# Optimization experiments

Measured on AMD Instinct MI355X. Metric: run time of the kernel, lower is better.

The kernel has to match this reference:

```python
import jax, jax.numpy as jnp
import numpy as np

B, GS, IN_H, GCN_H, LIN_H = 65536, 7, 5, 144, 128


def _xavier(key, shape):
    fan_in, fan_out = shape[0], shape[1]
    limit = np.sqrt(6.0 / (fan_in + fan_out)).astype(np.float32)
    return jax.random.uniform(key, shape, jnp.float32, -limit, limit)


def setup_inputs() -> dict:
    key = jax.random.key(0)
    ks = jax.random.split(key, 12)
    operations = jax.random.normal(ks[0], (B, GS, IN_H), jnp.float32)
    adjacency = (jax.random.uniform(ks[1], (B, GS, GS)) < 0.3).astype(jnp.float32)
    num_vertices = jax.random.randint(ks[2], (B,), 1, 8).astype(jnp.float32)
    w1_0 = _xavier(ks[3], (IN_H, GCN_H))
    w2_0 = _xavier(ks[4], (IN_H, GCN_H))
    w1_1 = _xavier(ks[5], (GCN_H, GCN_H))
    w2_1 = _xavier(ks[6], (GCN_H, GCN_H))
    w1_2 = _xavier(ks[7], (GCN_H, GCN_H))
    w2_2 = _xavier(ks[8], (GCN_H, GCN_H))
    fc1_w = _xavier(ks[9], (LIN_H, GCN_H))  # torch Linear stores [out, in]
    fc2_w = _xavier(ks[10], (1, LIN_H))
    return {
        'operations': operations, 'adjacency': adjacency, 'num_vertices': num_vertices,
        'w1_0': w1_0, 'w2_0': w2_0, 'w1_1': w1_1, 'w2_1': w2_1,
        'w1_2': w1_2, 'w2_2': w2_2, 'fc1_w': fc1_w, 'fc2_w': fc2_w,
    }


def _row_normalize(adj):
    # divide each row by its sum (matches torch normalize_adj)
    return adj / adj.sum(axis=2, keepdims=True)


def reference(operations, adjacency, num_vertices,
              w1_0, w2_0, w1_1, w2_1, w1_2, w2_2, fc1_w, fc2_w):
    gs = adjacency.shape[1]
    eye = jnp.eye(gs, dtype=adjacency.dtype)
    adj_d = _row_normalize(adjacency + eye)  # [B, gs, gs]
    x = operations
    for w1, w2 in ((w1_0, w2_0), (w1_1, w2_1), (w1_2, w2_2)):
        norm_adj = _row_normalize(adj_d)                      # identity in value, kept faithful
        inv_norm_adj = _row_normalize(adj_d.transpose(0, 2, 1))
        o1 = jax.nn.relu(jnp.einsum('bij,bjk->bik', norm_adj, x @ w1))
        o2 = jax.nn.relu(jnp.einsum('bij,bjk->bik', inv_norm_adj, x @ w2))
        x = (o1 + o2) * 0.5  # dropout is identity at inference
    pooled = x.sum(axis=1) / num_vertices[:, None]            # [B, gcn_hidden]
    h = pooled @ fc1_w.T                                      # [B, linear_hidden]
    out = (h @ fc2_w.T).reshape(-1)                           # [B]
    return out
```

## Files before the change

### kernel.cpp

```cpp
#include <hip/hip_runtime.h>


typedef _Float16 half8   __attribute__((ext_vector_type(8)));
typedef _Float16 half4_t __attribute__((ext_vector_type(4)));
typedef float    floatx16 __attribute__((ext_vector_type(16)));

constexpr int GS = 7;
constexpr int NI = 8;
constexpr int MROWS = NI * GS;
constexpr int H = 144;
constexpr int LSTRIDE = 2 * 5 * 9 * 512;
constexpr int WT_HALFS = 3 * LSTRIDE;
constexpr int FRAGS = 3 * 90 * 64;

static __device__ inline half8 bc(_Float16 v) {
    half8 h = {v, v, v, v, v, v, v, v};
    return h;
}

__global__ void prep_kernel(const float* __restrict__ w10, const float* __restrict__ w20,
                            const float* __restrict__ w11, const float* __restrict__ w21,
                            const float* __restrict__ w12, const float* __restrict__ w22,
                            const float* __restrict__ fc1, const float* __restrict__ fc2,
                            _Float16* __restrict__ wt, float* __restrict__ g)
{
    if (blockIdx.x == 68) {
        const int j = threadIdx.x;
        if (j < H) {
            float s = 0.f;
            for (int o = 0; o < 128; ++o) s = fmaf(fc2[o], fc1[o * H + j], s);
            g[j] = s;
        }
        return;
    }
    const int t = blockIdx.x * 256 + threadIdx.x;
    if (t >= FRAGS) return;
    const int l    = t / (90 * 64);
    const int r    = t - l * (90 * 64);
    const int frag = r >> 6;
    const int lane = r & 63;
    const int p    = frag / 45;
    const int rem  = frag - p * 45;
    const int nt   = rem / 9;
    const int ks   = rem - nt * 9;
    const int n    = nt * 32 + (lane & 31);
    const int k0   = ks * 16 + (lane >> 5) * 8;
    const float* W = (l == 0) ? (p ? w20 : w10)
                   : (l == 1) ? (p ? w21 : w11)
                              : (p ? w22 : w12);
    const int K = (l == 0) ? 5 : 144;
    half8 h = bc((_Float16)0);
    #pragma unroll
    for (int j = 0; j < 8; ++j) {
        const int k = k0 + j;
        if (n < H && k < K) h[j] = (_Float16)W[k * H + n];
    }
    *(half8*)(wt + (size_t)l * LSTRIDE + (size_t)frag * 512 + (size_t)lane * 8) = h;
}

template<int NK, int CB>
static __device__ __forceinline__ void layer_pass(const _Float16* __restrict__ wl,
                                                  const int tid, const int lane, const int wv,
                                                  _Float16 (*sX)[152],
                                                  _Float16 (*sXn)[152], _Float16 (*sXi)[152],
                                                  const _Float16 (*sAh)[2][GS][8])
{
    for (int u = tid; u < MROWS * CB; u += 256) {
        const int row = u / CB, cb = u - row * CB;
        const int item = row / GS, rr = row - item * GS;
        const int c0 = cb * 8;
        const half8 aN = *(const half8*)&sAh[item][0][rr][0];
        const half8 aI = *(const half8*)&sAh[item][1][rr][0];
        half8 an = bc((_Float16)0), ai = bc((_Float16)0);
        #pragma unroll
        for (int j = 0; j < GS; ++j) {
            const half8 xj = *(const half8*)&sX[item * GS + j][c0];
            an += bc(aN[j]) * xj;
            ai += bc(aI[j]) * xj;
        }
        *(half8*)&sXn[row][c0] = an;
        *(half8*)&sXi[row][c0] = ai;
    }
    __syncthreads();

    const int  nt    = wv;
    const bool extra = (wv >= 2);
    const int  em    = wv & 1;
    const int  khi   = (lane >> 5) * 8;
    const int  r0    = lane & 31;
    const int  r1    = 32 + r0;
    const int  r1c   = (r1 < MROWS) ? r1 : (MROWS - 1);

    floatx16 a1m0, a1m1, a2m0, a2m1, e1, e2;
    #pragma unroll
    for (int i = 0; i < 16; ++i) {
        a1m0[i] = 0.f; a1m1[i] = 0.f; a2m0[i] = 0.f; a2m1[i] = 0.f;
        e1[i] = 0.f; e2[i] = 0.f;
    }

    #pragma unroll
    for (int ks = 0; ks < NK; ++ks) {
        const int c = ks * 16 + khi;
        const half8 bn0 = *(const half8*)&sXn[r0][c];
        const half8 bn1 = *(const half8*)&sXn[r1c][c];
        const half8 bi0 = *(const half8*)&sXi[r0][c];
        const half8 bi1 = *(const half8*)&sXi[r1c][c];
        const _Float16* f1 = wl + (size_t)((nt * 9 + ks) * 512) + (size_t)lane * 8;
        const half8 A1 = *(const half8*)f1;
        const half8 A2 = *(const half8*)(f1 + 45 * 512);
        a1m0 = __builtin_amdgcn_mfma_f32_32x32x16_f16(A1, bn0, a1m0, 0, 0, 0);
        a1m1 = __builtin_amdgcn_mfma_f32_32x32x16_f16(A1, bn1, a1m1, 0, 0, 0);
        a2m0 = __builtin_amdgcn_mfma_f32_32x32x16_f16(A2, bi0, a2m0, 0, 0, 0);
        a2m1 = __builtin_amdgcn_mfma_f32_32x32x16_f16(A2, bi1, a2m1, 0, 0, 0);
        if (extra) {
            const _Float16* f4 = wl + (size_t)((36 + ks) * 512) + (size_t)lane * 8;
            const half8 E1 = *(const half8*)f4;
            const half8 E2 = *(const half8*)(f4 + 45 * 512);
            e1 = __builtin_amdgcn_mfma_f32_32x32x16_f16(E1, em ? bn1 : bn0, e1, 0, 0, 0);
            e2 = __builtin_amdgcn_mfma_f32_32x32x16_f16(E2, em ? bi1 : bi0, e2, 0, 0, 0);
        }
    }

    #pragma unroll
    for (int q = 0; q < 4; ++q) {
        const int n0 = nt * 32 + 4 * (lane >> 5) + 8 * q;
        half4_t h0, h1;
        #pragma unroll
        for (int i = 0; i < 4; ++i) {
            float v1 = a1m0[4 * q + i]; v1 = v1 > 0.f ? v1 : 0.f;
            float v2 = a2m0[4 * q + i]; v2 = v2 > 0.f ? v2 : 0.f;
            h0[i] = (_Float16)(0.5f * (v1 + v2));
            float w1 = a1m1[4 * q + i]; w1 = w1 > 0.f ? w1 : 0.f;
            float w2 = a2m1[4 * q + i]; w2 = w2 > 0.f ? w2 : 0.f;
            h1[i] = (_Float16)(0.5f * (w1 + w2));
        }
        *(half4_t*)&sX[r0][n0] = h0;
        if (r0 < MROWS - 32) *(half4_t*)&sX[r1][n0] = h1;
    }
    if (extra) {
        #pragma unroll
        for (int q = 0; q < 2; ++q) {
            const int n0 = 128 + 4 * (lane >> 5) + 8 * q;
            half4_t h;
            #pragma unroll
            for (int i = 0; i < 4; ++i) {
                float v1 = e1[4 * q + i]; v1 = v1 > 0.f ? v1 : 0.f;
                float v2 = e2[4 * q + i]; v2 = v2 > 0.f ? v2 : 0.f;
                h[i] = (_Float16)(0.5f * (v1 + v2));
            }
            const int rr = em * 32 + r0;
            if (rr < MROWS) *(half4_t*)&sX[rr][n0] = h;
        }
    }
    __syncthreads();
}

__global__ __launch_bounds__(256, 3)
void gcn_mfma(const float* __restrict__ ops, const float* __restrict__ adj,
              const float* __restrict__ nv,
              const _Float16* __restrict__ wt, const float* __restrict__ gw,
              float* __restrict__ out)
{
    __shared__ __align__(16) _Float16 sX [MROWS][152];
    __shared__ __align__(16) _Float16 sXn[MROWS][152];
    __shared__ __align__(16) _Float16 sXi[MROWS][152];
    __shared__ __align__(16) _Float16 sAh[NI][2][GS][8];

    float (*adjd)[GS][GS] = (float(*)[GS][GS])&sXn[0][0];

    const int tid  = threadIdx.x;
    const int lane = tid & 63;
    const int wv   = tid >> 6;
    const int ibase = blockIdx.x * NI;

    if (tid < MROWS) {
        const int item = tid / GS, r = tid % GS;
        const float* orow = ops + ((size_t)(ibase + item) * GS + r) * 5;
        half8 h = bc((_Float16)0);
        h[0] = (_Float16)orow[0]; h[1] = (_Float16)orow[1]; h[2] = (_Float16)orow[2];
        h[3] = (_Float16)orow[3]; h[4] = (_Float16)orow[4];
        *(half8*)&sX[tid][0] = h;
        *(half8*)&sX[tid][8] = bc((_Float16)0);

        const float* arow = adj + ((size_t)(ibase + item) * GS + r) * GS;
        float a[GS]; float sm = 0.f;
        #pragma unroll
        for (int c = 0; c < GS; ++c) { a[c] = arow[c] + (c == r ? 1.f : 0.f); sm += a[c]; }
        const float is = 1.f / sm;
        #pragma unroll
        for (int c = 0; c < GS; ++c) {
            const float v = a[c] * is;
            adjd[item][r][c] = v;
            sAh[item][0][r][c] = (_Float16)v;
        }
        sAh[item][0][r][7] = (_Float16)0.f;
    }
    __syncthreads();
    if (tid < MROWS) {
        const int item = tid / GS, r = tid % GS;
        float v[GS]; float sm = 0.f;
        #pragma unroll
        for (int k = 0; k < GS; ++k) { v[k] = adjd[item][k][r]; sm += v[k]; }
        const float is = 1.f / sm;
        #pragma unroll
        for (int k = 0; k < GS; ++k) sAh[item][1][r][k] = (_Float16)(v[k] * is);
        sAh[item][1][r][7] = (_Float16)0.f;
    }
    __syncthreads();

    layer_pass<1, 2>(wt,                        tid, lane, wv, sX, sXn, sXi, sAh);
    layer_pass<9, 18>(wt + (size_t)1 * LSTRIDE, tid, lane, wv, sX, sXn, sXi, sAh);
    layer_pass<9, 18>(wt + (size_t)2 * LSTRIDE, tid, lane, wv, sX, sXn, sXi, sAh);

    if (tid < NI * 16) {
        const int item = tid >> 4, part = tid & 15;
        float s = 0.f;
        #pragma unroll
        for (int c = 0; c < 9; ++c) {
            const int j = part * 9 + c;
            const float gj = gw[j];
            #pragma unroll
            for (int i = 0; i < GS; ++i)
                s = fmaf((float)sX[item * GS + i][j], gj, s);
        }
        s += __shfl_xor(s, 1);
        s += __shfl_xor(s, 2);
        s += __shfl_xor(s, 4);
        s += __shfl_xor(s, 8);
        if (part == 0) out[ibase + item] = s / nv[ibase + item];
    }
}

extern "C" void kernel_launch(void* const* d_in, const int* in_sizes, int n_in,
                              void* d_out, int out_size, void* d_ws, size_t ws_size,
                              hipStream_t stream) {
    const float* ops = (const float*)d_in[0];
    const float* adj = (const float*)d_in[1];
    const float* nv  = (const float*)d_in[2];
    const float* w10 = (const float*)d_in[3];
    const float* w20 = (const float*)d_in[4];
    const float* w11 = (const float*)d_in[5];
    const float* w21 = (const float*)d_in[6];
    const float* w12 = (const float*)d_in[7];
    const float* w22 = (const float*)d_in[8];
    const float* fc1 = (const float*)d_in[9];
    const float* fc2 = (const float*)d_in[10];

    _Float16* wt = (_Float16*)d_ws;
    float*    g  = (float*)((char*)d_ws + (size_t)WT_HALFS * 2);

    prep_kernel<<<69, 256, 0, stream>>>(w10, w20, w11, w21, w12, w22,
                                        fc1, fc2, wt, g);
    gcn_mfma<<<65536 / NI, 256, 0, stream>>>(ops, adj, nv, wt, g, (float*)d_out);
}
```

Baseline: 268.8 us.

## Halve items per block to one MFMA row tile and fold half-scale into weights

```diff
diff --git a/kernel.cpp b/kernel.cpp
--- a/kernel.cpp
+++ b/kernel.cpp
@@ -6,9 +6,10 @@
 typedef float    floatx16 __attribute__((ext_vector_type(16)));
 
 constexpr int GS = 7;
-constexpr int NI = 8;
+constexpr int NI = 4;
 constexpr int MROWS = NI * GS;
 constexpr int H = 144;
+constexpr int XS = 156;
 constexpr int LSTRIDE = 2 * 5 * 9 * 512;
 constexpr int WT_HALFS = 3 * LSTRIDE;
 constexpr int FRAGS = 3 * 90 * 64;
@@ -53,7 +54,7 @@
     #pragma unroll
     for (int j = 0; j < 8; ++j) {
         const int k = k0 + j;
-        if (n < H && k < K) h[j] = (_Float16)W[k * H + n];
+        if (n < H && k < K) h[j] = (_Float16)(0.5f * W[k * H + n]);
     }
     *(half8*)(wt + (size_t)l * LSTRIDE + (size_t)frag * 512 + (size_t)lane * 8) = h;
 }
@@ -61,8 +62,8 @@
 template<int NK, int CB>
 static __device__ __forceinline__ void layer_pass(const _Float16* __restrict__ wl,
                                                   const int tid, const int lane, const int wv,
-                                                  _Float16 (*sX)[152],
-                                                  _Float16 (*sXn)[152], _Float16 (*sXi)[152],
+                                                  _Float16 (*sX)[XS],
+                                                  _Float16 (*sXn)[XS], _Float16 (*sXi)[XS],
                                                   const _Float16 (*sAh)[2][GS][8])
 {
     for (int u = tid; u < MROWS * CB; u += 256) {
@@ -83,87 +84,79 @@
     }
     __syncthreads();
 
-    const int  nt    = wv;
-    const bool extra = (wv >= 2);
-    const int  em    = wv & 1;
-    const int  khi   = (lane >> 5) * 8;
-    const int  r0    = lane & 31;
-    const int  r1    = 32 + r0;
-    const int  r1c   = (r1 < MROWS) ? r1 : (MROWS - 1);
-
-    floatx16 a1m0, a1m1, a2m0, a2m1, e1, e2;
-    #pragma unroll
-    for (int i = 0; i < 16; ++i) {
-        a1m0[i] = 0.f; a1m1[i] = 0.f; a2m0[i] = 0.f; a2m1[i] = 0.f;
-        e1[i] = 0.f; e2[i] = 0.f;
-    }
-
-    #pragma unroll
-    for (int ks = 0; ks < NK; ++ks) {
-        const int c = ks * 16 + khi;
-        const half8 bn0 = *(const half8*)&sXn[r0][c];
-        const half8 bn1 = *(const half8*)&sXn[r1c][c];
-        const half8 bi0 = *(const half8*)&sXi[r0][c];
-        const half8 bi1 = *(const half8*)&sXi[r1c][c];
-        const _Float16* f1 = wl + (size_t)((nt * 9 + ks) * 512) + (size_t)lane * 8;
-        const half8 A1 = *(const half8*)f1;
-        const half8 A2 = *(const half8*)(f1 + 45 * 512);
-        a1m0 = __builtin_amdgcn_mfma_f32_32x32x16_f16(A1, bn0, a1m0, 0, 0, 0);
-        a1m1 = __builtin_amdgcn_mfma_f32_32x32x16_f16(A1, bn1, a1m1, 0, 0, 0);
-        a2m0 = __builtin_amdgcn_mfma_f32_32x32x16_f16(A2, bi0, a2m0, 0, 0, 0);
-        a2m1 = __builtin_amdgcn_mfma_f32_32x32x16_f16(A2, bi1, a2m1, 0, 0, 0);
-        if (extra) {
-            const _Float16* f4 = wl + (size_t)((36 + ks) * 512) + (size_t)lane * 8;
-            const half8 E1 = *(const half8*)f4;
-            const half8 E2 = *(const half8*)(f4 + 45 * 512);
-            e1 = __builtin_amdgcn_mfma_f32_32x32x16_f16(E1, em ? bn1 : bn0, e1, 0, 0, 0);
-            e2 = __builtin_amdgcn_mfma_f32_32x32x16_f16(E2, em ? bi1 : bi0, e2, 0, 0, 0);
-        }
-    }
-
-    #pragma unroll
-    for (int q = 0; q < 4; ++q) {
-        const int n0 = nt * 32 + 4 * (lane >> 5) + 8 * q;
-        half4_t h0, h1;
-        #pragma unroll
-        for (int i = 0; i < 4; ++i) {
-            float v1 = a1m0[4 * q + i]; v1 = v1 > 0.f ? v1 : 0.f;
-            float v2 = a2m0[4 * q + i]; v2 = v2 > 0.f ? v2 : 0.f;
-            h0[i] = (_Float16)(0.5f * (v1 + v2));
-            float w1 = a1m1[4 * q + i]; w1 = w1 > 0.f ? w1 : 0.f;
-            float w2 = a2m1[4 * q + i]; w2 = w2 > 0.f ? w2 : 0.f;
-            h1[i] = (_Float16)(0.5f * (w1 + w2));
-        }
-        *(half4_t*)&sX[r0][n0] = h0;
-        if (r0 < MROWS - 32) *(half4_t*)&sX[r1][n0] = h1;
-    }
-    if (extra) {
-        #pragma unroll
-        for (int q = 0; q < 2; ++q) {
-            const int n0 = 128 + 4 * (lane >> 5) + 8 * q;
-            half4_t h;
+    const int khi = (lane >> 5) * 8;
+    const int r0  = lane & 31;
+    const int rc  = (r0 < MROWS) ? r0 : (MROWS - 1);
+
+    {
+        floatx16 a1, a2;
+        #pragma unroll
+        for (int i = 0; i < 16; ++i) { a1[i] = 0.f; a2[i] = 0.f; }
+        #pragma unroll
+        for (int ks = 0; ks < NK; ++ks) {
+            const int c = ks * 16 + khi;
+            const half8 bn = *(const half8*)&sXn[rc][c];
+            const half8 bi = *(const half8*)&sXi[rc][c];
+            const _Float16* f = wl + (size_t)((wv * 9 + ks) * 512) + (size_t)lane * 8;
+            a1 = __builtin_amdgcn_mfma_f32_32x32x16_f16(*(const half8*)f,              bn, a1, 0, 0, 0);
+            a2 = __builtin_amdgcn_mfma_f32_32x32x16_f16(*(const half8*)(f + 45 * 512), bi, a2, 0, 0, 0);
+        }
+        if (r0 < MROWS) {
             #pragma unroll
-            for (int i = 0; i < 4; ++i) {
-                float v1 = e1[4 * q + i]; v1 = v1 > 0.f ? v1 : 0.f;
-                float v2 = e2[4 * q + i]; v2 = v2 > 0.f ? v2 : 0.f;
-                h[i] = (_Float16)(0.5f * (v1 + v2));
+            for (int q = 0; q < 4; ++q) {
+                const int n0 = wv * 32 + 4 * (lane >> 5) + 8 * q;
+                half4_t h;
+                #pragma unroll
+                for (int i = 0; i < 4; ++i) {
+                    float v1 = a1[4 * q + i]; v1 = v1 > 0.f ? v1 : 0.f;
+                    float v2 = a2[4 * q + i]; v2 = v2 > 0.f ? v2 : 0.f;
+                    h[i] = (_Float16)(v1 + v2);
+                }
+                *(half4_t*)&sX[r0][n0] = h;
             }
-            const int rr = em * 32 + r0;
-            if (rr < MROWS) *(half4_t*)&sX[rr][n0] = h;
-        }
-    }
-    __syncthreads();
-}
-
-__global__ __launch_bounds__(256, 3)
+        }
+    }
+
+    if (wv == 0) {
+        floatx16 e1, e2;
+        #pragma unroll
+        for (int i = 0; i < 16; ++i) { e1[i] = 0.f; e2[i] = 0.f; }
+        #pragma unroll
+        for (int ks = 0; ks < NK; ++ks) {
+            const int c = ks * 16 + khi;
+            const half8 bn = *(const half8*)&sXn[rc][c];
+            const half8 bi = *(const half8*)&sXi[rc][c];
+            const _Float16* f = wl + (size_t)((36 + ks) * 512) + (size_t)lane * 8;
+            e1 = __builtin_amdgcn_mfma_f32_32x32x16_f16(*(const half8*)f,              bn, e1, 0, 0, 0);
+            e2 = __builtin_amdgcn_mfma_f32_32x32x16_f16(*(const half8*)(f + 45 * 512), bi, e2, 0, 0, 0);
+        }
+        if (r0 < MROWS) {
+            #pragma unroll
+            for (int q = 0; q < 2; ++q) {
+                const int n0 = 128 + 4 * (lane >> 5) + 8 * q;
+                half4_t h;
+                #pragma unroll
+                for (int i = 0; i < 4; ++i) {
+                    float v1 = e1[4 * q + i]; v1 = v1 > 0.f ? v1 : 0.f;
+                    float v2 = e2[4 * q + i]; v2 = v2 > 0.f ? v2 : 0.f;
+                    h[i] = (_Float16)(v1 + v2);
+                }
+                *(half4_t*)&sX[r0][n0] = h;
+            }
+        }
+    }
+    __syncthreads();
+}
+
+__global__ __launch_bounds__(256, 5)
 void gcn_mfma(const float* __restrict__ ops, const float* __restrict__ adj,
               const float* __restrict__ nv,
               const _Float16* __restrict__ wt, const float* __restrict__ gw,
               float* __restrict__ out)
 {
-    __shared__ __align__(16) _Float16 sX [MROWS][152];
-    __shared__ __align__(16) _Float16 sXn[MROWS][152];
-    __shared__ __align__(16) _Float16 sXi[MROWS][152];
+    __shared__ __align__(16) _Float16 sX [MROWS][XS];
+    __shared__ __align__(16) _Float16 sXn[MROWS][XS];
+    __shared__ __align__(16) _Float16 sXi[MROWS][XS];
     __shared__ __align__(16) _Float16 sAh[NI][2][GS][8];
 
     float (*adjd)[GS][GS] = (float(*)[GS][GS])&sXn[0][0];
```

Measured after the change: 577.9 us. 115% more time.
